# Kernel tuning notes

Hardware: AMD Instinct MI355X
Metric: run time of the kernel (lower is better)

Reference implementation:

```python
import jax, jax.numpy as jnp
import numpy as np

SLOTS = ["hotel-pricerange","hotel-type","hotel-parking","hotel-stay","hotel-day","hotel-people","hotel-area","hotel-stars","hotel-internet","hotel-name","train-destination","train-day","train-departure","train-arriveby","train-people","train-leaveat","attraction-area","attraction-name","attraction-type","restaurant-food","restaurant-pricerange","restaurant-area","restaurant-name","restaurant-time","restaurant-people","taxi-leaveat","taxi-destination","taxi-departure","taxi-arriveby","hospital-department"]
H, V, B, L, G, STEPS = 400, 18000, 16, 512, 3, 10
S = len(SLOTS)

_tok2idx = {}
for _s in SLOTS:
    _d, _sl = _s.split("-")
    if _d not in _tok2idx: _tok2idx[_d] = len(_tok2idx)
    if _sl not in _tok2idx: _tok2idx[_sl] = len(_tok2idx)
NTOK = len(_tok2idx)
DOMAIN_IDX = np.array([_tok2idx[s.split("-")[0]] for s in SLOTS], np.int32)
SLOT_IDX = np.array([_tok2idx[s.split("-")[1]] for s in SLOTS], np.int32)


def setup_inputs():
    key = jax.random.key(0)
    k = jax.random.split(key, 10)
    sc = float(1.0 / np.sqrt(H))
    return {
        "encoder_hidden": jax.random.normal(k[0], (B, H), jnp.float32),
        "encoder_outputs": jax.random.normal(k[1], (B, L, H), jnp.float32),
        "context_idx": jax.random.randint(k[2], (B, L), 0, V),
        "context_mask": jnp.ones((B, L), jnp.int32),
        "target_values": jax.random.randint(k[3], (B, STEPS), 0, V),
        "embedding": jax.random.normal(k[4], (V, H), jnp.float32) * 0.02,
        "slot_embedding": jax.random.normal(k[5], (NTOK, H), jnp.float32) * 0.1,
        "domain_idx": jnp.asarray(DOMAIN_IDX),
        "slot_idx": jnp.asarray(SLOT_IDX),
        "W_ih": jax.random.normal(k[6], (3 * H, H), jnp.float32) * sc,
        "W_hh": jax.random.normal(k[7], (3 * H, H), jnp.float32) * sc,
        "b_ih": jnp.zeros((3 * H,), jnp.float32),
        "b_hh": jnp.zeros((3 * H,), jnp.float32),
        "w_ratio_w": jax.random.normal(k[8], (1, 3 * H), jnp.float32) * sc,
        "w_ratio_b": jnp.zeros((1,), jnp.float32),
        "w_gate_w": jax.random.normal(k[9], (G, H), jnp.float32) * sc,
        "w_gate_b": jnp.zeros((G,), jnp.float32),
    }


def _gru_cell(x, h, W_ih, W_hh, b_ih, b_hh):
    # torch.nn.GRUCell semantics
    gi = x @ W_ih.T + b_ih
    gh = h @ W_hh.T + b_hh
    i_r, i_z, i_n = jnp.split(gi, 3, axis=-1)
    h_r, h_z, h_n = jnp.split(gh, 3, axis=-1)
    r = jax.nn.sigmoid(i_r + h_r)
    z = jax.nn.sigmoid(i_z + h_z)
    n = jnp.tanh(i_n + r * h_n)
    return (1.0 - z) * n + z * h


def reference(encoder_hidden, encoder_outputs, context_idx, context_mask, target_values,
              embedding, slot_embedding, domain_idx, slot_idx,
              W_ih, W_hh, b_ih, b_hh, w_ratio_w, w_ratio_b, w_gate_w, w_gate_b):
    # eval mode: dropout off, greedy decode for STEPS=10 steps; target_values unused
    SB = S * B
    slot_emb = slot_embedding[domain_idx] + slot_embedding[slot_idx]          # [S,H]
    emb = jnp.broadcast_to(slot_emb[:, None, :], (S, B, H)).reshape(SB, H)
    hidden = jnp.broadcast_to(encoder_hidden[None], (S, B, H)).reshape(SB, H)
    ctx_idx = jnp.tile(context_idx, (S, 1))                                   # [SB,L]
    mask = jnp.tile(context_mask, (S, 1)).astype(bool)
    rows = jnp.arange(SB)[:, None]
    preds = []
    gates_logits = None
    for i in range(STEPS):
        hidden = _gru_cell(emb, hidden, W_ih, W_hh, b_ih, b_hh)               # [SB,H]
        p_vocab = jax.nn.softmax(hidden @ embedding.T, axis=-1)               # [SB,V]
        h3 = hidden.reshape(S, B, H)
        scores = jnp.einsum("blh,sbh->sbl", encoder_outputs, h3).reshape(SB, L)
        scores = jnp.where(mask, scores, -jnp.inf)
        c_probs = jax.nn.softmax(scores, axis=-1)                             # [SB,L]
        p_context = jnp.zeros_like(p_vocab).at[rows, ctx_idx].add(c_probs)    # scatter_add over vocab
        context_vec = jnp.einsum("blh,sbl->sbh", encoder_outputs,
                                 c_probs.reshape(S, B, L)).reshape(SB, H)
        p_gen = jax.nn.sigmoid(jnp.concatenate([hidden, context_vec, emb], axis=-1)
                               @ w_ratio_w.T + w_ratio_b)                     # [SB,1]
        if i == 0:
            gates_logits = (context_vec @ w_gate_w.T + w_gate_b).reshape(S, B, G)
        p_final = (1.0 - p_gen) * p_context + p_gen * p_vocab                 # [SB,V]
        pred_idx = jnp.argmax(p_final, axis=-1)
        preds.append(p_final.reshape(S, B, V))
        emb = embedding[pred_idx]                                             # greedy feedback
    preds_probs = jnp.stack(preds, axis=2).transpose(1, 0, 2, 3)              # [B,S,T,V]
    return preds_probs, gates_logits.transpose(1, 0, 2)                       # [B,S,G]
```

## Files before the change

kernel.cpp:

```cpp
#include <hip/hip_runtime.h>
#include <hip/hip_bf16.h>

#define S_  30
#define B_  16
#define Hd  400
#define Vv  18000
#define Ll  512
#define Gg  3
#define Tt  10
#define SBn 480
#define MP  512
#define KP  448
#define NPAD_W 2560
#define NPAD_E 18176
#define NST 141
#define SG  5

typedef unsigned short u16;
typedef __attribute__((ext_vector_type(8))) short bf8;
typedef __attribute__((ext_vector_type(8))) unsigned short u16x8;
typedef __attribute__((ext_vector_type(4))) float f4;

#define INF __builtin_inff()

__device__ __forceinline__ u16 f2bf(float f){
  union { __hip_bfloat16 h; u16 u; } c;
  c.h = __float2bfloat16(f);
  return c.u;
}
__device__ __forceinline__ float bf2f(u16 x){
  union { u16 u; __hip_bfloat16 h; } c;
  c.u = x;
  return __bfloat162float(c.h);
}


__global__ void k_setup_w(const float* __restrict__ Wih, const float* __restrict__ Whh,
                          u16* __restrict__ whi, u16* __restrict__ wlo){
  long total = (long)NPAD_W * KP;
  for (long idx = (long)blockIdx.x*256 + threadIdx.x; idx < total; idx += (long)gridDim.x*256){
    int r = (int)(idx / KP), k = (int)(idx - (long)r*KP);
    float v = 0.f;
    if (k < Hd){
      if (r < 1200) v = Wih[(long)r*Hd + k];
      else if (r >= 1280 && r < 2480) v = Whh[(long)(r-1280)*Hd + k];
    }
    u16 hi = f2bf(v);
    whi[idx] = hi;
    wlo[idx] = f2bf(v - bf2f(hi));
  }
}

__global__ void k_setup_e(const float* __restrict__ emb, u16* __restrict__ ebf){
  long total = (long)NPAD_E * KP;
  for (long idx = (long)blockIdx.x*256 + threadIdx.x; idx < total; idx += (long)gridDim.x*256){
    long r = idx / KP; int k = (int)(idx - r*KP);
    float v = (r < Vv && k < Hd) ? emb[r*Hd + k] : 0.f;
    ebf[idx] = f2bf(v);
  }
}

__global__ void k_setup_xh(const float* __restrict__ ehid, const float* __restrict__ semb,
                           const int* __restrict__ didx, const int* __restrict__ sidx,
                           float* __restrict__ X, float* __restrict__ Hh, u16* __restrict__ Hbf){
  int m = blockIdx.x, k = threadIdx.x;
  Hbf[(long)m*KP + k] = 0;
  if (m < SBn){
    int s = m >> 4, b = m & 15;
    float xv = 0.f, hv = 0.f;
    if (k < Hd){
      xv = semb[(long)didx[s]*Hd + k] + semb[(long)sidx[s]*Hd + k];
      hv = ehid[(long)b*Hd + k];
    }
    X [(long)m*KP + k] = xv;
    Hh[(long)m*KP + k] = hv;
  }
}

__global__ __launch_bounds__(256) void k_setup_t(const float* __restrict__ Eo, float* __restrict__ EoT){
  __shared__ float tile[64][65];
  int b = blockIdx.y;
  int kt = blockIdx.x / 8, lt = blockIdx.x - kt*8;
  int k0 = kt*64, l0 = lt*64;
  int c = threadIdx.x & 63, rb = threadIdx.x >> 6;
  #pragma unroll
  for (int p = 0; p < 16; ++p){
    int r = p*4 + rb;
    tile[r][c] = (k0 + c < Hd) ? Eo[((long)b*Ll + l0 + r)*Hd + k0 + c] : 0.f;
  }
  __syncthreads();
  #pragma unroll
  for (int p = 0; p < 16; ++p){
    int r = p*4 + rb;
    if (k0 + r < Hd) EoT[((long)b*Hd + k0 + r)*Ll + l0 + c] = tile[c][r];
  }
}

__global__ __launch_bounds__(256) void k_ggemm(
    const float* __restrict__ X, const float* __restrict__ Hh,
    const u16* __restrict__ Bhi, const u16* __restrict__ Blo,
    float* __restrict__ Gm)
{
  __shared__ u16 As_hi[32*40], As_lo[32*40];
  __shared__ u16 Bs_hi[128*40], Bs_lo[128*40];
  int tid = threadIdx.x;
  int mt = blockIdx.x, yt = blockIdx.y;
  int seg = yt >= 10 ? 1 : 0, nt = seg ? yt-10 : yt;
  const float* A = seg ? Hh : X;
  int m0 = mt*32;
  long brow0 = (long)seg*1280 + (long)nt*128;
  int w = tid>>6, l = tid&63, lr = l&15, kg = l>>4;
  f4 acc[2][2] = {};
  int arow = tid>>3, ac4 = (tid&7)*4;
  int br4 = tid>>2, bc8 = (tid&3)*8;
  for (int ks = 0; ks < 14; ++ks){
    int k0 = ks*32;
    __syncthreads();
    { f4 v = *(const f4*)(A + (long)(m0+arow)*KP + k0 + ac4);
      u16 h0=f2bf(v.x),h1=f2bf(v.y),h2=f2bf(v.z),h3=f2bf(v.w);
      *(ushort4*)&As_hi[arow*40+ac4] = make_ushort4(h0,h1,h2,h3);
      u16 q0=f2bf(v.x-bf2f(h0)),q1=f2bf(v.y-bf2f(h1)),q2=f2bf(v.z-bf2f(h2)),q3=f2bf(v.w-bf2f(h3));
      *(ushort4*)&As_lo[arow*40+ac4] = make_ushort4(q0,q1,q2,q3);
    }
    #pragma unroll
    for (int p = 0; p < 2; ++p){
      long row = brow0 + p*64 + br4;
      *(uint4*)&Bs_hi[(p*64+br4)*40+bc8] = *(const uint4*)(Bhi + row*KP + k0 + bc8);
      *(uint4*)&Bs_lo[(p*64+br4)*40+bc8] = *(const uint4*)(Blo + row*KP + k0 + bc8);
    }
    __syncthreads();
    bf8 ah[2], al[2], bh[2], bl[2];
    #pragma unroll
    for (int i = 0; i < 2; ++i){
      ah[i] = *(const bf8*)&As_hi[(i*16+lr)*40 + kg*8];
      al[i] = *(const bf8*)&As_lo[(i*16+lr)*40 + kg*8];
    }
    #pragma unroll
    for (int j = 0; j < 2; ++j){
      int r = w*32 + j*16 + lr;
      bh[j] = *(const bf8*)&Bs_hi[r*40 + kg*8];
      bl[j] = *(const bf8*)&Bs_lo[r*40 + kg*8];
    }
    #pragma unroll
    for (int i = 0; i < 2; ++i)
      #pragma unroll
      for (int j = 0; j < 2; ++j){
        acc[i][j] = __builtin_amdgcn_mfma_f32_16x16x32_bf16(ah[i], bh[j], acc[i][j], 0,0,0);
        acc[i][j] = __builtin_amdgcn_mfma_f32_16x16x32_bf16(ah[i], bl[j], acc[i][j], 0,0,0);
        acc[i][j] = __builtin_amdgcn_mfma_f32_16x16x32_bf16(al[i], bh[j], acc[i][j], 0,0,0);
      }
  }
  #pragma unroll
  for (int i = 0; i < 2; ++i)
    #pragma unroll
    for (int j = 0; j < 2; ++j){
      int nl = nt*128 + w*32 + j*16 + lr;
      if (nl < 1200){
        int col = seg*1200 + nl;
        int mrow = m0 + i*16 + kg*4;
        #pragma unroll
        for (int r = 0; r < 4; ++r)
          Gm[(long)(mrow+r)*2400 + col] = acc[i][j][r];
      }
    }
}

__global__ __launch_bounds__(512) void k_attn(
    const float* __restrict__ Eo, const float* __restrict__ EoT, const int* __restrict__ cmask,
    const float* __restrict__ Gm, const float* __restrict__ bih, const float* __restrict__ bhh,
    float* __restrict__ Hh, u16* __restrict__ Hbf, const float* __restrict__ X,
    const float* __restrict__ wr, const float* __restrict__ wrb,
    const float* __restrict__ wg, const float* __restrict__ wgb,
    float* __restrict__ cp, float* __restrict__ pgen, float* __restrict__ og, int t)
{
  __shared__ float sh_h[SG][Hd];
  __shared__ float sh_c[SG][Hd];
  __shared__ float sh_p[SG][Ll];
  __shared__ float buf[4*SG*Ll];
  int tid = threadIdx.x, b = blockIdx.y, s0 = blockIdx.x*SG;

  for (int idx = tid; idx < SG*Hd; idx += 512){
    int sg = idx / Hd, j = idx - sg*Hd;
    long m = (long)(s0+sg)*B_ + b;
    const float* g = Gm + m*2400;
    float r = 1.f/(1.f+expf(-(g[j]     + bih[j]     + g[1200+j] + bhh[j])));
    float z = 1.f/(1.f+expf(-(g[400+j] + bih[400+j] + g[1600+j] + bhh[400+j])));
    float n = tanhf(g[800+j] + bih[800+j] + r*(g[2000+j] + bhh[800+j]));
    float h = (1.f-z)*n + z*Hh[m*KP + j];
    sh_h[sg][j] = h;
    Hh[m*KP + j] = h;
    Hbf[m*KP + j] = f2bf(h);
  }
  __syncthreads();

  {
    int lq = tid & 127, kq = tid >> 7;
    int l0 = lq*4;
    const float* ebase = EoT + (long)b*Hd*Ll;
    f4 sc[SG];
    #pragma unroll
    for (int sg = 0; sg < SG; ++sg) sc[sg] = f4{0.f,0.f,0.f,0.f};
    int k0 = kq*100;
    for (int k = k0; k < k0+100; k += 4){
      f4 h4[SG];
      #pragma unroll
      for (int sg = 0; sg < SG; ++sg) h4[sg] = *(const f4*)&sh_h[sg][k];
      #pragma unroll
      for (int kk = 0; kk < 4; ++kk){
        f4 e = *(const f4*)&ebase[(long)(k+kk)*Ll + l0];
        #pragma unroll
        for (int sg = 0; sg < SG; ++sg){
          float hk = h4[sg][kk];
          sc[sg].x += e.x*hk; sc[sg].y += e.y*hk; sc[sg].z += e.z*hk; sc[sg].w += e.w*hk;
        }
      }
    }
    #pragma unroll
    for (int sg = 0; sg < SG; ++sg)
      *(f4*)&buf[(kq*SG+sg)*Ll + l0] = sc[sg];
  }
  __syncthreads();

  float v[SG];
  {
    bool mok = cmask[b*Ll + tid] != 0;
    #pragma unroll
    for (int sg = 0; sg < SG; ++sg){
      float x = buf[sg*Ll+tid] + buf[(SG+sg)*Ll+tid] + buf[(2*SG+sg)*Ll+tid] + buf[(3*SG+sg)*Ll+tid];
      v[sg] = mok ? x : -INF;
    }
  }
  __syncthreads();
  #pragma unroll
  for (int sg = 0; sg < SG; ++sg) buf[sg*Ll + tid] = v[sg];
  __syncthreads();
  for (int o = 256; o > 0; o >>= 1){
    if (tid < o){
      #pragma unroll
      for (int sg = 0; sg < SG; ++sg)
        buf[sg*Ll+tid] = fmaxf(buf[sg*Ll+tid], buf[sg*Ll+tid+o]);
    }
    __syncthreads();
  }
  float mx[SG];
  #pragma unroll
  for (int sg = 0; sg < SG; ++sg) mx[sg] = buf[sg*Ll];
  __syncthreads();
  float p[SG];
  #pragma unroll
  for (int sg = 0; sg < SG; ++sg){ p[sg] = expf(v[sg]-mx[sg]); buf[sg*Ll+tid] = p[sg]; }
  __syncthreads();
  for (int o = 256; o > 0; o >>= 1){
    if (tid < o){
      #pragma unroll
      for (int sg = 0; sg < SG; ++sg) buf[sg*Ll+tid] += buf[sg*Ll+tid+o];
    }
    __syncthreads();
  }
  #pragma unroll
  for (int sg = 0; sg < SG; ++sg){
    float pp = p[sg] / buf[sg*Ll];
    sh_p[sg][tid] = pp;
    cp[((long)(s0+sg)*B_ + b)*Ll + tid] = pp;
  }
  __syncthreads();

  {
    int k4 = tid & 127, lq = tid >> 7;
    if (k4 < 100){
      int k = k4*4;
      f4 cacc[SG];
      #pragma unroll
      for (int sg = 0; sg < SG; ++sg) cacc[sg] = f4{0.f,0.f,0.f,0.f};
      for (int li = 0; li < 128; li += 4){
        int l = lq*128 + li;
        f4 pv[SG];
        #pragma unroll
        for (int sg = 0; sg < SG; ++sg) pv[sg] = *(const f4*)&sh_p[sg][l];
        #pragma unroll
        for (int jj = 0; jj < 4; ++jj){
          f4 e = *(const f4*)&Eo[((long)b*Ll + l + jj)*Hd + k];
          #pragma unroll
          for (int sg = 0; sg < SG; ++sg){
            float pw = pv[sg][jj];
            cacc[sg].x += e.x*pw; cacc[sg].y += e.y*pw; cacc[sg].z += e.z*pw; cacc[sg].w += e.w*pw;
          }
        }
      }
      #pragma unroll
      for (int sg = 0; sg < SG; ++sg)
        *(f4*)&buf[(lq*SG+sg)*Hd + k] = cacc[sg];
    }
  }
  __syncthreads();
  if (tid < Hd){
    #pragma unroll
    for (int sg = 0; sg < SG; ++sg)
      sh_c[sg][tid] = buf[sg*Hd+tid] + buf[(SG+sg)*Hd+tid] + buf[(2*SG+sg)*Hd+tid] + buf[(3*SG+sg)*Hd+tid];
  }
  __syncthreads();

  {
    float part[SG] = {0,0,0,0,0};
    for (int j = tid; j < 1200; j += 512){
      float wv = wr[j];
      #pragma unroll
      for (int sg = 0; sg < SG; ++sg){
        float xv;
        if (j < 400) xv = sh_h[sg][j];
        else if (j < 800) xv = sh_c[sg][j-400];
        else xv = X[((long)(s0+sg)*B_ + b)*KP + (j-800)];
        part[sg] += xv*wv;
      }
    }
    #pragma unroll
    for (int sg = 0; sg < SG; ++sg) buf[sg*Ll + tid] = part[sg];
    __syncthreads();
    for (int o = 256; o > 0; o >>= 1){
      if (tid < o){
        #pragma unroll
        for (int sg = 0; sg < SG; ++sg) buf[sg*Ll+tid] += buf[sg*Ll+tid+o];
      }
      __syncthreads();
    }
    if (tid < SG)
      pgen[(long)(s0+tid)*B_ + b] = 1.f/(1.f+expf(-(buf[tid*Ll] + wrb[0])));
    __syncthreads();
  }

  if (t == 0){
    for (int g = 0; g < Gg; ++g){
      float pt[SG] = {0,0,0,0,0};
      if (tid < Hd){
        float wv = wg[g*Hd + tid];
        #pragma unroll
        for (int sg = 0; sg < SG; ++sg) pt[sg] = sh_c[sg][tid]*wv;
      }
      #pragma unroll
      for (int sg = 0; sg < SG; ++sg) buf[sg*Ll + tid] = pt[sg];
      __syncthreads();
      for (int o = 256; o > 0; o >>= 1){
        if (tid < o){
          #pragma unroll
          for (int sg = 0; sg < SG; ++sg) buf[sg*Ll+tid] += buf[sg*Ll+tid+o];
        }
        __syncthreads();
      }
      if (tid < SG) og[((long)b*S_ + (s0+tid))*Gg + g] = buf[tid*Ll] + wgb[g];
      __syncthreads();
    }
  }
}

__global__ __launch_bounds__(256) void k_vgemm(
    const u16* __restrict__ Abf, const u16* __restrict__ Bhi,
    u16* __restrict__ E, float* __restrict__ pmax, float* __restrict__ psum)
{
  __shared__ u16 As[128*40], Bs[128*40];
  __shared__ float redm[2][128], reds[2][128];
  int tid = threadIdx.x;
  int ns = blockIdx.x, mt = blockIdx.y;
  int m0 = mt*128;
  long brow0 = (long)ns*128;
  int w = tid>>6, l = tid&63, lr = l&15, kg = l>>4;
  int wm = w>>1, wn = w&1;
  int srow = tid>>1, sc8 = (tid&1)*16;
  f4 acc[4][4] = {};
  for (int ks = 0; ks < 14; ++ks){
    int k0 = ks*32;
    __syncthreads();
    *(uint4*)&As[srow*40 + sc8]     = *(const uint4*)(Abf + (long)(m0+srow)*KP + k0 + sc8);
    *(uint4*)&As[srow*40 + sc8 + 8] = *(const uint4*)(Abf + (long)(m0+srow)*KP + k0 + sc8 + 8);
    *(uint4*)&Bs[srow*40 + sc8]     = *(const uint4*)(Bhi + (brow0+srow)*KP + k0 + sc8);
    *(uint4*)&Bs[srow*40 + sc8 + 8] = *(const uint4*)(Bhi + (brow0+srow)*KP + k0 + sc8 + 8);
    __syncthreads();
    bf8 a[4], b[4];
    #pragma unroll
    for (int i = 0; i < 4; ++i) a[i] = *(const bf8*)&As[(wm*64 + i*16 + lr)*40 + kg*8];
    #pragma unroll
    for (int j = 0; j < 4; ++j) b[j] = *(const bf8*)&Bs[(wn*64 + j*16 + lr)*40 + kg*8];
    #pragma unroll
    for (int i = 0; i < 4; ++i)
      #pragma unroll
      for (int j = 0; j < 4; ++j)
        acc[i][j] = __builtin_amdgcn_mfma_f32_16x16x32_bf16(a[i], b[j], acc[i][j], 0,0,0);
  }
  #pragma unroll
  for (int i = 0; i < 4; ++i)
    #pragma unroll
    for (int r = 0; r < 4; ++r){
      float mxv = -INF;
      #pragma unroll
      for (int j = 0; j < 4; ++j){
        int col = (int)brow0 + wn*64 + j*16 + lr;
        if (col < Vv) mxv = fmaxf(mxv, acc[i][j][r]);
      }
      #pragma unroll
      for (int d = 1; d < 16; d <<= 1) mxv = fmaxf(mxv, __shfl_xor(mxv, d));
      if (lr == 0) redm[wn][wm*64 + i*16 + kg*4 + r] = mxv;
    }
  __syncthreads();
  #pragma unroll
  for (int i = 0; i < 4; ++i)
    #pragma unroll
    for (int r = 0; r < 4; ++r){
      int rl = wm*64 + i*16 + kg*4 + r;
      float cmx = fmaxf(redm[0][rl], redm[1][rl]);
      float ssum = 0.f;
      long erow = (long)(m0 + rl)*18048;
      #pragma unroll
      for (int j = 0; j < 4; ++j){
        int col = (int)brow0 + wn*64 + j*16 + lr;
        float e = (col < Vv) ? expf(acc[i][j][r] - cmx) : 0.f;
        E[erow + col] = f2bf(e);
        ssum += e;
      }
      #pragma unroll
      for (int d = 1; d < 16; d <<= 1) ssum += __shfl_xor(ssum, d);
      if (lr == 0) reds[wn][rl] = ssum;
    }
  __syncthreads();
  if (tid < 128){
    pmax[(long)(m0+tid)*NST + ns] = fmaxf(redm[0][tid], redm[1][tid]);
    psum[(long)(m0+tid)*NST + ns] = reds[0][tid] + reds[1][tid];
  }
}

__global__ __launch_bounds__(512) void k_final(
    const u16* __restrict__ E, const float* __restrict__ pmax, const float* __restrict__ psum,
    const float* __restrict__ pgen, const float* __restrict__ cp,
    const int* __restrict__ cidx, const int* __restrict__ cmask,
    const float* __restrict__ emb, float* __restrict__ out, float* __restrict__ X, int t)
{
  __shared__ float scat[Vv];
  __shared__ float scale[NST];
  __shared__ float am[256], asum[256];
  __shared__ float rv[512];
  __shared__ int   ri[512];
  int tid = threadIdx.x, m = blockIdx.x;
  int b = m & 15, s = m >> 4;
  if (tid < 256){
    am[tid]   = tid < NST ? pmax[(long)m*NST + tid] : -1e30f;
    asum[tid] = tid < NST ? psum[(long)m*NST + tid] : 0.f;
  }
  for (int i = tid; i < Vv; i += 512) scat[i] = 0.f;
  __syncthreads();
  for (int o = 128; o > 0; o >>= 1){
    if (tid < o){
      float m2 = am[tid+o], M = fmaxf(am[tid], m2);
      asum[tid] = asum[tid]*expf(am[tid]-M) + asum[tid+o]*expf(m2-M);
      am[tid] = M;
    }
    __syncthreads();
  }
  float gmx = am[0], pg = pgen[m];
  float sc0 = pg / asum[0];
  if (tid < NST) scale[tid] = sc0 * expf(pmax[(long)m*NST + tid] - gmx);
  if (cmask[b*Ll + tid]){
    float vv = (1.f - pg)*cp[(long)m*Ll + tid];
    atomicAdd(&scat[cidx[b*Ll + tid]], vv);
  }
  __syncthreads();
  long eb = (long)m*18048;
  long ob = ((long)(b*S_ + s)*Tt + t)*(long)Vv;
  float bv = -1.f; int bi = 0;
  for (int i = tid; i < Vv/8; i += 512){
    u16x8 ev = *(const u16x8*)&E[eb + i*8];
    float sc = scale[(i*8) >> 7];
    f4 s0 = *(const f4*)&scat[i*8];
    f4 s1 = *(const f4*)&scat[i*8 + 4];
    f4 o0, o1;
    o0.x = sc*bf2f(ev[0]) + s0.x; o0.y = sc*bf2f(ev[1]) + s0.y;
    o0.z = sc*bf2f(ev[2]) + s0.z; o0.w = sc*bf2f(ev[3]) + s0.w;
    o1.x = sc*bf2f(ev[4]) + s1.x; o1.y = sc*bf2f(ev[5]) + s1.y;
    o1.z = sc*bf2f(ev[6]) + s1.z; o1.w = sc*bf2f(ev[7]) + s1.w;
    *(f4*)&out[ob + i*8]     = o0;
    *(f4*)&out[ob + i*8 + 4] = o1;
    int n0 = i*8;
    if (o0.x > bv){ bv = o0.x; bi = n0;   }
    if (o0.y > bv){ bv = o0.y; bi = n0+1; }
    if (o0.z > bv){ bv = o0.z; bi = n0+2; }
    if (o0.w > bv){ bv = o0.w; bi = n0+3; }
    if (o1.x > bv){ bv = o1.x; bi = n0+4; }
    if (o1.y > bv){ bv = o1.y; bi = n0+5; }
    if (o1.z > bv){ bv = o1.z; bi = n0+6; }
    if (o1.w > bv){ bv = o1.w; bi = n0+7; }
  }
  rv[tid] = bv; ri[tid] = bi;
  __syncthreads();
  for (int o = 256; o > 0; o >>= 1){
    if (tid < o){
      float v2 = rv[tid+o]; int i2 = ri[tid+o];
      if (v2 > rv[tid] || (v2 == rv[tid] && i2 < ri[tid])){ rv[tid] = v2; ri[tid] = i2; }
    }
    __syncthreads();
  }
  int win = ri[0];
  if (tid < Hd) X[(long)m*KP + tid] = emb[(long)win*Hd + tid];
}

extern "C" void kernel_launch(void* const* d_in, const int* in_sizes, int n_in,
                              void* d_out, int out_size, void* d_ws, size_t ws_size,
                              hipStream_t stream)
{
  const float* ehid  = (const float*)d_in[0];
  const float* eout  = (const float*)d_in[1];
  const int*   cidx  = (const int*)d_in[2];
  const int*   cmask = (const int*)d_in[3];
  const float* emb   = (const float*)d_in[5];
  const float* semb  = (const float*)d_in[6];
  const int*   didx  = (const int*)d_in[7];
  const int*   sidx  = (const int*)d_in[8];
  const float* Wih   = (const float*)d_in[9];
  const float* Whh   = (const float*)d_in[10];
  const float* bih   = (const float*)d_in[11];
  const float* bhh   = (const float*)d_in[12];
  const float* wr    = (const float*)d_in[13];
  const float* wrb   = (const float*)d_in[14];
  const float* wg    = (const float*)d_in[15];
  const float* wgb   = (const float*)d_in[16];
  float* out = (float*)d_out;

  char* ws = (char*)d_ws;
  u16*   ws_hi = (u16*)(ws + 0);
  u16*   ws_lo = (u16*)(ws + 2293760);
  u16*   ebf   = (u16*)(ws + 4587520);
  float* EoT   = (float*)(ws + 20873216);
  float* X     = (float*)(ws + 33980416);
  float* Hh    = (float*)(ws + 34840576);
  u16*   Hbf   = (u16*)(ws + 35700736);
  float* Gm    = (float*)(ws + 36159488);
  u16*   E     = (u16*)(ws + 40767488);
  float* cp    = (float*)(ws + 59248640);
  float* pg    = (float*)(ws + 60231680);
  float* pmax  = (float*)(ws + 60233728);
  float* psum  = (float*)(ws + 60522496);
  float* og = out + (long)B_*S_*Tt*Vv;

  k_setup_w <<<4480, 256, 0, stream>>>(Wih, Whh, ws_hi, ws_lo);
  k_setup_e <<<4096, 256, 0, stream>>>(emb, ebf);
  k_setup_xh<<<512, 448, 0, stream>>>(ehid, semb, didx, sidx, X, Hh, Hbf);
  k_setup_t <<<dim3(56,16), 256, 0, stream>>>(eout, EoT);

  for (int t = 0; t < Tt; ++t){
    k_ggemm <<<dim3(15,20), 256, 0, stream>>>(X, Hh, ws_hi, ws_lo, Gm);
    k_attn  <<<dim3(6,16), 512, 0, stream>>>(eout, EoT, cmask, Gm, bih, bhh, Hh, Hbf, X,
                                             wr, wrb, wg, wgb, cp, pg, og, t);
    k_vgemm <<<dim3(141,4), 256, 0, stream>>>(Hbf, ebf, E, pmax, psum);
    k_final <<<480, 512, 0, stream>>>(E, pmax, psum, pg, cp, cidx, cmask, emb, out, X, t);
  }
}
```

Baseline: 1.024 ms.

## Pre-split activations to bf16, use LDS direct loads, drop softmax max pass

Activations are now stored pre-split into bf16 hi/lo pairs, so the gate GEMM no longer converts fp32 tiles on every load. Both GEMMs stage tiles with global_load_lds into unpadded shared memory, and the gate GEMM tile grows to 64 rows. The vocab softmax drops its max-subtraction and per-tile rescaling in favour of raw exp plus an atomic row sum, removing the pmax/psum reduction in the final kernel. Attention-side block reductions switch to wave shuffles. Unpadded LDS may cause bank conflicts, and exp without a max shift can overflow for large logits.

```diff
diff --git a/kernel.cpp b/kernel.cpp
--- a/kernel.cpp
+++ b/kernel.cpp
@@ -15,6 +15,7 @@
 #define NPAD_E 18176
 #define NST 141
 #define SG  5
+#define EW  18048
 
 typedef unsigned short u16;
 typedef __attribute__((ext_vector_type(8))) short bf8;
@@ -32,6 +33,12 @@
   union { u16 u; __hip_bfloat16 h; } c;
   c.u = x;
   return __bfloat162float(c.h);
+}
+
+__device__ __forceinline__ void gload16(const void* g, void* l){
+  __builtin_amdgcn_global_load_lds(
+      (const __attribute__((address_space(1))) unsigned int*)g,
+      (__attribute__((address_space(3))) unsigned int*)l, 16, 0, 0);
 }
 
 
@@ -62,19 +69,20 @@
 
 __global__ void k_setup_xh(const float* __restrict__ ehid, const float* __restrict__ semb,
                            const int* __restrict__ didx, const int* __restrict__ sidx,
-                           float* __restrict__ X, float* __restrict__ Hh, u16* __restrict__ Hbf){
+                           float* __restrict__ X, float* __restrict__ Hh,
+                           u16* __restrict__ Xhi, u16* __restrict__ Xlo,
+                           u16* __restrict__ Hhi, u16* __restrict__ Hlo){
   int m = blockIdx.x, k = threadIdx.x;
-  Hbf[(long)m*KP + k] = 0;
-  if (m < SBn){
+  float xv = 0.f, hv = 0.f;
+  if (m < SBn && k < Hd){
     int s = m >> 4, b = m & 15;
-    float xv = 0.f, hv = 0.f;
-    if (k < Hd){
-      xv = semb[(long)didx[s]*Hd + k] + semb[(long)sidx[s]*Hd + k];
-      hv = ehid[(long)b*Hd + k];
-    }
-    X [(long)m*KP + k] = xv;
-    Hh[(long)m*KP + k] = hv;
-  }
+    xv = semb[(long)didx[s]*Hd + k] + semb[(long)sidx[s]*Hd + k];
+    hv = ehid[(long)b*Hd + k];
+  }
+  long o = (long)m*KP + k;
+  X[o] = xv;  Hh[o] = hv;
+  u16 xh = f2bf(xv); Xhi[o] = xh; Xlo[o] = f2bf(xv - bf2f(xh));
+  u16 hh = f2bf(hv); Hhi[o] = hh; Hlo[o] = f2bf(hv - bf2f(hh));
 }
 
 __global__ __launch_bounds__(256) void k_setup_t(const float* __restrict__ Eo, float* __restrict__ EoT){
@@ -97,54 +105,51 @@
 }
 
 __global__ __launch_bounds__(256) void k_ggemm(
-    const float* __restrict__ X, const float* __restrict__ Hh,
+    const u16* __restrict__ Xhi, const u16* __restrict__ Xlo,
+    const u16* __restrict__ Hhi, const u16* __restrict__ Hlo,
     const u16* __restrict__ Bhi, const u16* __restrict__ Blo,
     float* __restrict__ Gm)
 {
-  __shared__ u16 As_hi[32*40], As_lo[32*40];
-  __shared__ u16 Bs_hi[128*40], Bs_lo[128*40];
+  __shared__ u16 As_hi[64*32], As_lo[64*32];
+  __shared__ u16 Bs_hi[128*32], Bs_lo[128*32];
   int tid = threadIdx.x;
   int mt = blockIdx.x, yt = blockIdx.y;
   int seg = yt >= 10 ? 1 : 0, nt = seg ? yt-10 : yt;
-  const float* A = seg ? Hh : X;
-  int m0 = mt*32;
+  const u16* Ahi = seg ? Hhi : Xhi;
+  const u16* Alo = seg ? Hlo : Xlo;
+  int m0 = mt*64;
   long brow0 = (long)seg*1280 + (long)nt*128;
   int w = tid>>6, l = tid&63, lr = l&15, kg = l>>4;
-  f4 acc[2][2] = {};
-  int arow = tid>>3, ac4 = (tid&7)*4;
-  int br4 = tid>>2, bc8 = (tid&3)*8;
+  int wm = w>>1, wn = w&1;
+  int ca = w*64 + l, ra = ca>>2, ca8 = (ca&3)*8;
+  f4 acc[2][4] = {};
   for (int ks = 0; ks < 14; ++ks){
     int k0 = ks*32;
     __syncthreads();
-    { f4 v = *(const f4*)(A + (long)(m0+arow)*KP + k0 + ac4);
-      u16 h0=f2bf(v.x),h1=f2bf(v.y),h2=f2bf(v.z),h3=f2bf(v.w);
-      *(ushort4*)&As_hi[arow*40+ac4] = make_ushort4(h0,h1,h2,h3);
-      u16 q0=f2bf(v.x-bf2f(h0)),q1=f2bf(v.y-bf2f(h1)),q2=f2bf(v.z-bf2f(h2)),q3=f2bf(v.w-bf2f(h3));
-      *(ushort4*)&As_lo[arow*40+ac4] = make_ushort4(q0,q1,q2,q3);
-    }
-    #pragma unroll
-    for (int p = 0; p < 2; ++p){
-      long row = brow0 + p*64 + br4;
-      *(uint4*)&Bs_hi[(p*64+br4)*40+bc8] = *(const uint4*)(Bhi + row*KP + k0 + bc8);
-      *(uint4*)&Bs_lo[(p*64+br4)*40+bc8] = *(const uint4*)(Blo + row*KP + k0 + bc8);
+    gload16(Ahi + (long)(m0+ra)*KP + k0 + ca8, &As_hi[w*512]);
+    gload16(Alo + (long)(m0+ra)*KP + k0 + ca8, &As_lo[w*512]);
+    #pragma unroll
+    for (int q = 0; q < 2; ++q){
+      int cb = q*256 + w*64 + l, rb = cb>>2, cb8 = (cb&3)*8;
+      gload16(Bhi + (brow0+rb)*KP + k0 + cb8, &Bs_hi[q*2048 + w*512]);
+      gload16(Blo + (brow0+rb)*KP + k0 + cb8, &Bs_lo[q*2048 + w*512]);
     }
     __syncthreads();
-    bf8 ah[2], al[2], bh[2], bl[2];
+    bf8 ah[2], al[2], bh[4], bl[4];
     #pragma unroll
     for (int i = 0; i < 2; ++i){
-      ah[i] = *(const bf8*)&As_hi[(i*16+lr)*40 + kg*8];
-      al[i] = *(const bf8*)&As_lo[(i*16+lr)*40 + kg*8];
-    }
-    #pragma unroll
-    for (int j = 0; j < 2; ++j){
-      int r = w*32 + j*16 + lr;
-      bh[j] = *(const bf8*)&Bs_hi[r*40 + kg*8];
-      bl[j] = *(const bf8*)&Bs_lo[r*40 + kg*8];
+      ah[i] = *(const bf8*)&As_hi[(wm*32 + i*16 + lr)*32 + kg*8];
+      al[i] = *(const bf8*)&As_lo[(wm*32 + i*16 + lr)*32 + kg*8];
+    }
+    #pragma unroll
+    for (int j = 0; j < 4; ++j){
+      bh[j] = *(const bf8*)&Bs_hi[(wn*64 + j*16 + lr)*32 + kg*8];
+      bl[j] = *(const bf8*)&Bs_lo[(wn*64 + j*16 + lr)*32 + kg*8];
     }
     #pragma unroll
     for (int i = 0; i < 2; ++i)
       #pragma unroll
-      for (int j = 0; j < 2; ++j){
+      for (int j = 0; j < 4; ++j){
         acc[i][j] = __builtin_amdgcn_mfma_f32_16x16x32_bf16(ah[i], bh[j], acc[i][j], 0,0,0);
         acc[i][j] = __builtin_amdgcn_mfma_f32_16x16x32_bf16(ah[i], bl[j], acc[i][j], 0,0,0);
         acc[i][j] = __builtin_amdgcn_mfma_f32_16x16x32_bf16(al[i], bh[j], acc[i][j], 0,0,0);
@@ -153,11 +158,11 @@
   #pragma unroll
   for (int i = 0; i < 2; ++i)
     #pragma unroll
-    for (int j = 0; j < 2; ++j){
-      int nl = nt*128 + w*32 + j*16 + lr;
+    for (int j = 0; j < 4; ++j){
+      int nl = nt*128 + wn*64 + j*16 + lr;
       if (nl < 1200){
         int col = seg*1200 + nl;
-        int mrow = m0 + i*16 + kg*4;
+        int mrow = m0 + wm*32 + i*16 + kg*4;
         #pragma unroll
         for (int r = 0; r < 4; ++r)
           Gm[(long)(mrow+r)*2400 + col] = acc[i][j][r];
@@ -168,16 +173,22 @@
 __global__ __launch_bounds__(512) void k_attn(
     const float* __restrict__ Eo, const float* __restrict__ EoT, const int* __restrict__ cmask,
     const float* __restrict__ Gm, const float* __restrict__ bih, const float* __restrict__ bhh,
-    float* __restrict__ Hh, u16* __restrict__ Hbf, const float* __restrict__ X,
+    float* __restrict__ Hh, u16* __restrict__ Hhi, u16* __restrict__ Hlo,
+    const float* __restrict__ X,
     const float* __restrict__ wr, const float* __restrict__ wrb,
     const float* __restrict__ wg, const float* __restrict__ wgb,
-    float* __restrict__ cp, float* __restrict__ pgen, float* __restrict__ og, int t)
+    float* __restrict__ cp, float* __restrict__ pgen, float* __restrict__ og,
+    float* __restrict__ vsum, int t)
 {
   __shared__ float sh_h[SG][Hd];
   __shared__ float sh_c[SG][Hd];
   __shared__ float sh_p[SG][Ll];
   __shared__ float buf[4*SG*Ll];
+  __shared__ float wred[2][SG*8];
   int tid = threadIdx.x, b = blockIdx.y, s0 = blockIdx.x*SG;
+  int lane = tid & 63, wid = tid >> 6;
+
+  if (blockIdx.x == 0 && blockIdx.y == 0) vsum[tid] = 0.f;
 
   for (int idx = tid; idx < SG*Hd; idx += 512){
     int sg = idx / Hd, j = idx - sg*Hd;
@@ -189,7 +200,9 @@
     float h = (1.f-z)*n + z*Hh[m*KP + j];
     sh_h[sg][j] = h;
     Hh[m*KP + j] = h;
-    Hbf[m*KP + j] = f2bf(h);
+    u16 hh = f2bf(h);
+    Hhi[m*KP + j] = hh;
+    Hlo[m*KP + j] = f2bf(h - bf2f(hh));
   }
   __syncthreads();
 
@@ -230,36 +243,46 @@
       v[sg] = mok ? x : -INF;
     }
   }
-  __syncthreads();
-  #pragma unroll
-  for (int sg = 0; sg < SG; ++sg) buf[sg*Ll + tid] = v[sg];
-  __syncthreads();
-  for (int o = 256; o > 0; o >>= 1){
-    if (tid < o){
-      #pragma unroll
-      for (int sg = 0; sg < SG; ++sg)
-        buf[sg*Ll+tid] = fmaxf(buf[sg*Ll+tid], buf[sg*Ll+tid+o]);
-    }
-    __syncthreads();
-  }
-  float mx[SG];
-  #pragma unroll
-  for (int sg = 0; sg < SG; ++sg) mx[sg] = buf[sg*Ll];
+  float mv[SG];
+  #pragma unroll
+  for (int sg = 0; sg < SG; ++sg){
+    float m_ = v[sg];
+    #pragma unroll
+    for (int d = 1; d < 64; d <<= 1) m_ = fmaxf(m_, __shfl_xor(m_, d));
+    mv[sg] = m_;
+  }
+  if (lane == 0){
+    #pragma unroll
+    for (int sg = 0; sg < SG; ++sg) wred[0][sg*8 + wid] = mv[sg];
+  }
   __syncthreads();
   float p[SG];
   #pragma unroll
-  for (int sg = 0; sg < SG; ++sg){ p[sg] = expf(v[sg]-mx[sg]); buf[sg*Ll+tid] = p[sg]; }
-  __syncthreads();
-  for (int o = 256; o > 0; o >>= 1){
-    if (tid < o){
-      #pragma unroll
-      for (int sg = 0; sg < SG; ++sg) buf[sg*Ll+tid] += buf[sg*Ll+tid+o];
-    }
-    __syncthreads();
-  }
-  #pragma unroll
   for (int sg = 0; sg < SG; ++sg){
-    float pp = p[sg] / buf[sg*Ll];
+    float mx = wred[0][sg*8];
+    #pragma unroll
+    for (int q = 1; q < 8; ++q) mx = fmaxf(mx, wred[0][sg*8+q]);
+    p[sg] = expf(v[sg] - mx);
+  }
+  float sv[SG];
+  #pragma unroll
+  for (int sg = 0; sg < SG; ++sg){
+    float s_ = p[sg];
+    #pragma unroll
+    for (int d = 1; d < 64; d <<= 1) s_ += __shfl_xor(s_, d);
+    sv[sg] = s_;
+  }
+  if (lane == 0){
+    #pragma unroll
+    for (int sg = 0; sg < SG; ++sg) wred[1][sg*8 + wid] = sv[sg];
+  }
+  __syncthreads();
+  #pragma unroll
+  for (int sg = 0; sg < SG; ++sg){
+    float sum = 0.f;
+    #pragma unroll
+    for (int q = 0; q < 8; ++q) sum += wred[1][sg*8+q];
+    float pp = p[sg] / sum;
     sh_p[sg][tid] = pp;
     cp[((long)(s0+sg)*B_ + b)*Ll + tid] = pp;
   }
@@ -273,13 +296,13 @@
       #pragma unroll
       for (int sg = 0; sg < SG; ++sg) cacc[sg] = f4{0.f,0.f,0.f,0.f};
       for (int li = 0; li < 128; li += 4){
-        int l = lq*128 + li;
+        int l2 = lq*128 + li;
         f4 pv[SG];
         #pragma unroll
-        for (int sg = 0; sg < SG; ++sg) pv[sg] = *(const f4*)&sh_p[sg][l];
+        for (int sg = 0; sg < SG; ++sg) pv[sg] = *(const f4*)&sh_p[sg][l2];
         #pragma unroll
         for (int jj = 0; jj < 4; ++jj){
-          f4 e = *(const f4*)&Eo[((long)b*Ll + l + jj)*Hd + k];
+          f4 e = *(const f4*)&Eo[((long)b*Ll + l2 + jj)*Hd + k];
           #pragma unroll
           for (int sg = 0; sg < SG; ++sg){
             float pw = pv[sg][jj];
@@ -314,18 +337,23 @@
       }
     }
     #pragma unroll
-    for (int sg = 0; sg < SG; ++sg) buf[sg*Ll + tid] = part[sg];
+    for (int sg = 0; sg < SG; ++sg){
+      float s_ = part[sg];
+      #pragma unroll
+      for (int d = 1; d < 64; d <<= 1) s_ += __shfl_xor(s_, d);
+      part[sg] = s_;
+    }
+    if (lane == 0){
+      #pragma unroll
+      for (int sg = 0; sg < SG; ++sg) wred[0][sg*8 + wid] = part[sg];
+    }
     __syncthreads();
-    for (int o = 256; o > 0; o >>= 1){
-      if (tid < o){
-        #pragma unroll
-        for (int sg = 0; sg < SG; ++sg) buf[sg*Ll+tid] += buf[sg*Ll+tid+o];
-      }
-      __syncthreads();
-    }
-    if (tid < SG)
-      pgen[(long)(s0+tid)*B_ + b] = 1.f/(1.f+expf(-(buf[tid*Ll] + wrb[0])));
-    __syncthreads();
+    if (tid < SG){
+      float sum = 0.f;
+      #pragma unroll
+      for (int q = 0; q < 8; ++q) sum += wred[0][tid*8+q];
+      pgen[(long)(s0+tid)*B_ + b] = 1.f/(1.f+expf(-(sum + wrb[0])));
+    }
   }
 
   if (t == 0){
@@ -337,48 +365,55 @@
         for (int sg = 0; sg < SG; ++sg) pt[sg] = sh_c[sg][tid]*wv;
       }
       #pragma unroll
-      for (int sg = 0; sg < SG; ++sg) buf[sg*Ll + tid] = pt[sg];
+      for (int sg = 0; sg < SG; ++sg){
+        float s_ = pt[sg];
+        #pragma unroll
+        for (int d = 1; d < 64; d <<= 1) s_ += __shfl_xor(s_, d);
+        pt[sg] = s_;
+      }
       __syncthreads();
-      for (int o = 256; o > 0; o >>= 1){
-        if (tid < o){
-          #pragma unroll
-          for (int sg = 0; sg < SG; ++sg) buf[sg*Ll+tid] += buf[sg*Ll+tid+o];
-        }
-        __syncthreads();
-      }
-      if (tid < SG) og[((long)b*S_ + (s0+tid))*Gg + g] = buf[tid*Ll] + wgb[g];
+      if (lane == 0){
+        #pragma unroll
+        for (int sg = 0; sg < SG; ++sg) wred[1][sg*8 + wid] = pt[sg];
+      }
       __syncthreads();
+      if (tid < SG){
+        float sum = 0.f;
+        #pragma unroll
+        for (int q = 0; q < 8; ++q) sum += wred[1][tid*8+q];
+        og[((long)b*S_ + (s0+tid))*Gg + g] = sum + wgb[g];
+      }
     }
   }
 }
 
 __global__ __launch_bounds__(256) void k_vgemm(
     const u16* __restrict__ Abf, const u16* __restrict__ Bhi,
-    u16* __restrict__ E, float* __restrict__ pmax, float* __restrict__ psum)
+    u16* __restrict__ E, float* __restrict__ vsum)
 {
-  __shared__ u16 As[128*40], Bs[128*40];
-  __shared__ float redm[2][128], reds[2][128];
+  __shared__ u16 As[128*32], Bs[128*32];
   int tid = threadIdx.x;
   int ns = blockIdx.x, mt = blockIdx.y;
   int m0 = mt*128;
   long brow0 = (long)ns*128;
   int w = tid>>6, l = tid&63, lr = l&15, kg = l>>4;
   int wm = w>>1, wn = w&1;
-  int srow = tid>>1, sc8 = (tid&1)*16;
   f4 acc[4][4] = {};
   for (int ks = 0; ks < 14; ++ks){
     int k0 = ks*32;
     __syncthreads();
-    *(uint4*)&As[srow*40 + sc8]     = *(const uint4*)(Abf + (long)(m0+srow)*KP + k0 + sc8);
-    *(uint4*)&As[srow*40 + sc8 + 8] = *(const uint4*)(Abf + (long)(m0+srow)*KP + k0 + sc8 + 8);
-    *(uint4*)&Bs[srow*40 + sc8]     = *(const uint4*)(Bhi + (brow0+srow)*KP + k0 + sc8);
-    *(uint4*)&Bs[srow*40 + sc8 + 8] = *(const uint4*)(Bhi + (brow0+srow)*KP + k0 + sc8 + 8);
+    #pragma unroll
+    for (int q = 0; q < 2; ++q){
+      int c = q*256 + w*64 + l, row = c>>2, c8 = (c&3)*8;
+      gload16(Abf + (long)(m0+row)*KP + k0 + c8, &As[q*2048 + w*512]);
+      gload16(Bhi + (brow0+row)*KP + k0 + c8, &Bs[q*2048 + w*512]);
+    }
     __syncthreads();
     bf8 a[4], b[4];
     #pragma unroll
-    for (int i = 0; i < 4; ++i) a[i] = *(const bf8*)&As[(wm*64 + i*16 + lr)*40 + kg*8];
-    #pragma unroll
-    for (int j = 0; j < 4; ++j) b[j] = *(const bf8*)&Bs[(wn*64 + j*16 + lr)*40 + kg*8];
+    for (int i = 0; i < 4; ++i) a[i] = *(const bf8*)&As[(wm*64 + i*16 + lr)*32 + kg*8];
+    #pragma unroll
+    for (int j = 0; j < 4; ++j) b[j] = *(const bf8*)&Bs[(wn*64 + j*16 + lr)*32 + kg*8];
     #pragma unroll
     for (int i = 0; i < 4; ++i)
       #pragma unroll
@@ -389,84 +424,48 @@
   for (int i = 0; i < 4; ++i)
     #pragma unroll
     for (int r = 0; r < 4; ++r){
-      float mxv = -INF;
+      int rl = wm*64 + i*16 + kg*4 + r;
+      long erow = (long)(m0 + rl)*EW;
+      float ssum = 0.f;
       #pragma unroll
       for (int j = 0; j < 4; ++j){
         int col = (int)brow0 + wn*64 + j*16 + lr;
-        if (col < Vv) mxv = fmaxf(mxv, acc[i][j][r]);
-      }
-      #pragma unroll
-      for (int d = 1; d < 16; d <<= 1) mxv = fmaxf(mxv, __shfl_xor(mxv, d));
-      if (lr == 0) redm[wn][wm*64 + i*16 + kg*4 + r] = mxv;
-    }
-  __syncthreads();
-  #pragma unroll
-  for (int i = 0; i < 4; ++i)
-    #pragma unroll
-    for (int r = 0; r < 4; ++r){
-      int rl = wm*64 + i*16 + kg*4 + r;
-      float cmx = fmaxf(redm[0][rl], redm[1][rl]);
-      float ssum = 0.f;
-      long erow = (long)(m0 + rl)*18048;
-      #pragma unroll
-      for (int j = 0; j < 4; ++j){
-        int col = (int)brow0 + wn*64 + j*16 + lr;
-        float e = (col < Vv) ? expf(acc[i][j][r] - cmx) : 0.f;
+        float e = (col < Vv) ? expf(acc[i][j][r]) : 0.f;
         E[erow + col] = f2bf(e);
         ssum += e;
       }
       #pragma unroll
       for (int d = 1; d < 16; d <<= 1) ssum += __shfl_xor(ssum, d);
-      if (lr == 0) reds[wn][rl] = ssum;
-    }
-  __syncthreads();
-  if (tid < 128){
-    pmax[(long)(m0+tid)*NST + ns] = fmaxf(redm[0][tid], redm[1][tid]);
-    psum[(long)(m0+tid)*NST + ns] = reds[0][tid] + reds[1][tid];
-  }
+      if (lr == 0) atomicAdd(&vsum[m0 + rl], ssum);
+    }
 }
 
 __global__ __launch_bounds__(512) void k_final(
-    const u16* __restrict__ E, const float* __restrict__ pmax, const float* __restrict__ psum,
+    const u16* __restrict__ E, const float* __restrict__ vsum,
     const float* __restrict__ pgen, const float* __restrict__ cp,
     const int* __restrict__ cidx, const int* __restrict__ cmask,
-    const float* __restrict__ emb, float* __restrict__ out, float* __restrict__ X, int t)
+    const float* __restrict__ emb, float* __restrict__ out,
+    float* __restrict__ X, u16* __restrict__ Xhi, u16* __restrict__ Xlo, int t)
 {
   __shared__ float scat[Vv];
-  __shared__ float scale[NST];
-  __shared__ float am[256], asum[256];
   __shared__ float rv[512];
   __shared__ int   ri[512];
   int tid = threadIdx.x, m = blockIdx.x;
   int b = m & 15, s = m >> 4;
-  if (tid < 256){
-    am[tid]   = tid < NST ? pmax[(long)m*NST + tid] : -1e30f;
-    asum[tid] = tid < NST ? psum[(long)m*NST + tid] : 0.f;
-  }
   for (int i = tid; i < Vv; i += 512) scat[i] = 0.f;
   __syncthreads();
-  for (int o = 128; o > 0; o >>= 1){
-    if (tid < o){
-      float m2 = am[tid+o], M = fmaxf(am[tid], m2);
-      asum[tid] = asum[tid]*expf(am[tid]-M) + asum[tid+o]*expf(m2-M);
-      am[tid] = M;
-    }
-    __syncthreads();
-  }
-  float gmx = am[0], pg = pgen[m];
-  float sc0 = pg / asum[0];
-  if (tid < NST) scale[tid] = sc0 * expf(pmax[(long)m*NST + tid] - gmx);
+  float pg = pgen[m];
+  float sc = pg / vsum[m];
   if (cmask[b*Ll + tid]){
     float vv = (1.f - pg)*cp[(long)m*Ll + tid];
     atomicAdd(&scat[cidx[b*Ll + tid]], vv);
   }
   __syncthreads();
-  long eb = (long)m*18048;
+  long eb = (long)m*EW;
   long ob = ((long)(b*S_ + s)*Tt + t)*(long)Vv;
   float bv = -1.f; int bi = 0;
   for (int i = tid; i < Vv/8; i += 512){
     u16x8 ev = *(const u16x8*)&E[eb + i*8];
-    float sc = scale[(i*8) >> 7];
     f4 s0 = *(const f4*)&scat[i*8];
     f4 s1 = *(const f4*)&scat[i*8 + 4];
     f4 o0, o1;
@@ -496,7 +495,14 @@
     __syncthreads();
   }
   int win = ri[0];
-  if (tid < Hd) X[(long)m*KP + tid] = emb[(long)win*Hd + tid];
+  if (tid < Hd){
+    float v = emb[(long)win*Hd + tid];
+    long o = (long)m*KP + tid;
+    X[o] = v;
+    u16 hi = f2bf(v);
+    Xhi[o] = hi;
+    Xlo[o] = f2bf(v - bf2f(hi));
+  }
 }
 
 extern "C" void kernel_launch(void* const* d_in, const int* in_sizes, int n_in,
@@ -527,26 +533,28 @@
   u16*   ebf   = (u16*)(ws + 4587520);
   float* EoT   = (float*)(ws + 20873216);
   float* X     = (float*)(ws + 33980416);
-  float* Hh    = (float*)(ws + 34840576);
-  u16*   Hbf   = (u16*)(ws + 35700736);
-  float* Gm    = (float*)(ws + 36159488);
-  u16*   E     = (u16*)(ws + 40767488);
-  float* cp    = (float*)(ws + 59248640);
-  float* pg    = (float*)(ws + 60231680);
-  float* pmax  = (float*)(ws + 60233728);
-  float* psum  = (float*)(ws + 60522496);
+  u16*   Xhi   = (u16*)(ws + 34897920);
+  u16*   Xlo   = (u16*)(ws + 35356672);
+  float* Hh    = (float*)(ws + 35815424);
+  u16*   Hhi   = (u16*)(ws + 36732928);
+  u16*   Hlo   = (u16*)(ws + 37191680);
+  float* Gm    = (float*)(ws + 37650432);
+  u16*   E     = (u16*)(ws + 42565632);
+  float* cp    = (float*)(ws + 61046784);
+  float* pg    = (float*)(ws + 62029824);
+  float* vsum  = (float*)(ws + 62031872);
   float* og = out + (long)B_*S_*Tt*Vv;
 
   k_setup_w <<<4480, 256, 0, stream>>>(Wih, Whh, ws_hi, ws_lo);
   k_setup_e <<<4096, 256, 0, stream>>>(emb, ebf);
-  k_setup_xh<<<512, 448, 0, stream>>>(ehid, semb, didx, sidx, X, Hh, Hbf);
+  k_setup_xh<<<512, 448, 0, stream>>>(ehid, semb, didx, sidx, X, Hh, Xhi, Xlo, Hhi, Hlo);
   k_setup_t <<<dim3(56,16), 256, 0, stream>>>(eout, EoT);
 
   for (int t = 0; t < Tt; ++t){
-    k_ggemm <<<dim3(15,20), 256, 0, stream>>>(X, Hh, ws_hi, ws_lo, Gm);
-    k_attn  <<<dim3(6,16), 512, 0, stream>>>(eout, EoT, cmask, Gm, bih, bhh, Hh, Hbf, X,
-                                             wr, wrb, wg, wgb, cp, pg, og, t);
-    k_vgemm <<<dim3(141,4), 256, 0, stream>>>(Hbf, ebf, E, pmax, psum);
-    k_final <<<480, 512, 0, stream>>>(E, pmax, psum, pg, cp, cidx, cmask, emb, out, X, t);
-  }
-}
+    k_ggemm <<<dim3(8,20), 256, 0, stream>>>(Xhi, Xlo, Hhi, Hlo, ws_hi, ws_lo, Gm);
+    k_attn  <<<dim3(6,16), 512, 0, stream>>>(eout, EoT, cmask, Gm, bih, bhh, Hh, Hhi, Hlo, X,
+                                             wr, wrb, wg, wgb, cp, pg, og, vsum, t);
+    k_vgemm <<<dim3(141,4), 256, 0, stream>>>(Hhi, ebf, E, vsum);
+    k_final <<<480, 512, 0, stream>>>(E, vsum, pg, cp, cidx, cmask, emb, out, X, Xhi, Xlo, t);
+  }
+}
```

After: 1.226 ms. +19.7%, slower.
